# Kernel tuning notes

Hardware: AMD Instinct MI355X
Metric: run time of the kernel (lower is better)

Reference implementation:

```python
import jax, jax.numpy as jnp
from jax import lax
import numpy as np

B, T, D, H = 256, 512, 512, 1024

def _glorot(key, shape):
    fan_in, fan_out = shape
    lim = np.sqrt(6.0 / (fan_in + fan_out)).astype(np.float32)
    return jax.random.uniform(key, shape, jnp.float32, -lim, lim)

def setup_inputs() -> dict:
    key = jax.random.key(0)
    ks = jax.random.split(key, 7)
    return {
        "x": jax.random.normal(ks[0], (B, T, D), jnp.float32),
        "W": _glorot(ks[1], (D, H)),
        "U": _glorot(ks[2], (H, H)),
        "W_z": _glorot(ks[3], (D, H)),
        "U_z": _glorot(ks[4], (H, H)),
        "W_r": _glorot(ks[5], (D, H)),
        "U_r": _glorot(ks[6], (H, H)),
        "b": jnp.zeros((H,), jnp.float32),
        "b_z": jnp.zeros((H,), jnp.float32),
        "b_r": jnp.zeros((H,), jnp.float32),
    }

def reference(x, W, U, W_z, U_z, W_r, U_r, b, b_z, b_r):
    # GRU recurrence, faithful to source: update uses (1-z)*h + z*h_cand.
    def step(h, x_t):  # h: [B,H], x_t: [B,D]
        z = jax.nn.sigmoid(x_t @ W_z + h @ U_z + b_z)
        r = jax.nn.sigmoid(x_t @ W_r + h @ U_r + b_r)
        h_cand = jnp.tanh(x_t @ W + (r * h) @ U + b)
        h_new = (1.0 - z) * h + z * h_cand
        return h_new, None
    h0 = jnp.zeros((x.shape[0], W.shape[1]), x.dtype)
    xs = jnp.swapaxes(x, 0, 1)  # [T,B,D]
    hT, _ = lax.scan(step, h0, xs)
    return hT[:, None, :]  # [B,1,H] as in source (expand_dims kept through loop)
```

## Files before the change

### kernel.cpp

```cpp
#include <hip/hip_runtime.h>

typedef unsigned short ushort_t;
typedef __attribute__((ext_vector_type(8))) short short8;
typedef __attribute__((ext_vector_type(4))) float f32x4;
typedef __attribute__((ext_vector_type(4))) int i32x4;

#define NB   256
#define NT   512
#define ND   512
#define NH   1024
#define KK   1536
#define BK   128

__device__ __forceinline__ ushort_t f2bf(float f) {
  union { float f; unsigned u; } v; v.f = f;
  unsigned u = v.u;
  return (ushort_t)((u + 0x7FFFu + ((u >> 16) & 1u)) >> 16);
}
__device__ __forceinline__ int pack2(float a, float b) {
  return (int)(((unsigned)f2bf(b) << 16) | (unsigned)f2bf(a));
}
__device__ __forceinline__ float bf2f(ushort_t h) {
  union { unsigned u; float f; } v; v.u = ((unsigned)h) << 16; return v.f;
}
__device__ __forceinline__ float sigmoidf_(float x) {
  return 1.f / (1.f + __expf(-x));
}
__device__ __forceinline__ float tanhf_(float x) {
  return 1.f - 2.f / (__expf(2.f * x) + 1.f);
}

__global__ void repackT(const float* __restrict__ src, ushort_t* __restrict__ dst,
                        int K) {
  __shared__ float tile[64][65];
  const int k0 = blockIdx.x * 64, n0 = blockIdx.y * 64;
  const int tid = threadIdx.x;
  for (int i = 0; i < 16; ++i) {
    int e = tid + i * 256;
    int r = e >> 6, c = e & 63;
    tile[r][c] = src[(size_t)(k0 + r) * 1024 + n0 + c];
  }
  __syncthreads();
  for (int i = 0; i < 2; ++i) {
    int cch = tid + i * 256;
    int nl = cch >> 3, kc = (cch & 7) * 8;
    ushort_t tmp[8];
#pragma unroll
    for (int j = 0; j < 8; ++j) tmp[j] = f2bf(tile[kc + j][nl]);
    *reinterpret_cast<i32x4*>(dst + (size_t)(n0 + nl) * K + k0 + kc) =
        *reinterpret_cast<i32x4*>(tmp);
  }
}

__global__ void init_state(ushort_t* __restrict__ hb, float* __restrict__ hf) {
  int i = blockIdx.x * 256 + threadIdx.x;
  if (i < NB * NH) { hb[i] = 0; hf[i] = 0.f; }
}

__global__ void __launch_bounds__(256)
gxgemm(const float* __restrict__ x, const ushort_t* __restrict__ Bx,
       const float* __restrict__ bz, const float* __restrict__ br,
       const float* __restrict__ bb, ushort_t* __restrict__ Gx) {
  __shared__ __align__(16) char smem[32768];
  const int tid  = threadIdx.x;
  const int m0   = blockIdx.x * 64;
  const int n0   = blockIdx.y * 64;
  const int lane = tid & 63;
  const int w    = tid >> 6;
  const int wm   = w >> 1, wn = w & 1;
  const int l15  = lane & 15, l4 = lane >> 4;

  f32x4 acc[2][2];
#pragma unroll
  for (int i = 0; i < 2; ++i)
#pragma unroll
    for (int j = 0; j < 2; ++j) acc[i][j] = (f32x4){0.f, 0.f, 0.f, 0.f};

  for (int kb = 0; kb < 4; ++kb) {
    const int kbase = kb * BK;
#pragma unroll
    for (int i = 0; i < 4; ++i) {
      int c = tid + (i << 8);
      int r = c >> 4, kc = (c & 15) << 3;
      int m = m0 + r;
      int tt = m >> 8, b = m & 255;
      const float* xp = x + ((size_t)b * NT + tt) * ND + kbase + kc;
      f32x4 f0 = *reinterpret_cast<const f32x4*>(xp);
      f32x4 f1 = *reinterpret_cast<const f32x4*>(xp + 4);
      i32x4 v;
      v[0] = pack2(f0[0], f0[1]); v[1] = pack2(f0[2], f0[3]);
      v[2] = pack2(f1[0], f1[1]); v[3] = pack2(f1[2], f1[3]);
      int off = (r << 8) + (((kc << 1)) ^ ((r & 7) << 4));
      *reinterpret_cast<i32x4*>(&smem[off]) = v;
    }
#pragma unroll
    for (int i = 0; i < 4; ++i) {
      int c = tid + (i << 8);
      int n = c >> 4, kc = (c & 15) << 3;
      i32x4 v = *reinterpret_cast<const i32x4*>(Bx + (size_t)(n0 + n) * 512 + kbase + kc);
      int off = 16384 + (n << 8) + (((kc << 1)) ^ ((n & 7) << 4));
      *reinterpret_cast<i32x4*>(&smem[off]) = v;
    }
    __syncthreads();
#pragma unroll
    for (int ks = 0; ks < 4; ++ks) {
      int kbyte = ks * 64 + l4 * 16;
      short8 a[2], b[2];
#pragma unroll
      for (int i = 0; i < 2; ++i) {
        int ra = wm * 32 + i * 16 + l15;
        a[i] = *reinterpret_cast<short8*>(&smem[(ra << 8) + (kbyte ^ ((ra & 7) << 4))]);
        int nb = wn * 32 + i * 16 + l15;
        b[i] = *reinterpret_cast<short8*>(&smem[16384 + (nb << 8) + (kbyte ^ ((nb & 7) << 4))]);
      }
#pragma unroll
      for (int i = 0; i < 2; ++i)
#pragma unroll
        for (int j = 0; j < 2; ++j)
          acc[i][j] = __builtin_amdgcn_mfma_f32_16x16x32_bf16(a[i], b[j], acc[i][j], 0, 0, 0);
    }
    __syncthreads();
  }
#pragma unroll
  for (int i = 0; i < 2; ++i)
#pragma unroll
    for (int j = 0; j < 2; ++j) {
      int col = n0 + wn * 32 + j * 16 + l15;
      float bias = (col < NH) ? bz[col] : (col < 2 * NH ? br[col - NH] : bb[col - 2 * NH]);
      int mr = m0 + wm * 32 + i * 16 + 4 * l4;
#pragma unroll
      for (int jj = 0; jj < 4; ++jj)
        Gx[(size_t)(mr + jj) * 3072 + col] = f2bf(acc[i][j][jj] + bias);
    }
}

__global__ void __launch_bounds__(512)
p1k3(const ushort_t* __restrict__ Bu1, const ushort_t* __restrict__ hb,
     ushort_t* __restrict__ rhb, const float* __restrict__ hf,
     float* __restrict__ zfb, const ushort_t* __restrict__ Gx, int t) {
  extern __shared__ __align__(16) char dsm[];
  const int tid  = threadIdx.x;
  const int bid  = blockIdx.x;
  const int lane = tid & 63;
  const int w    = tid >> 6;
  const int l15  = lane & 15, l4 = lane >> 4;
  const int nt   = bid & 31;
  const int mt   = bid >> 5;
  const int m0   = mt * 32;
  const int n1   = nt * 64;
  const int msub = w >> 2, nsub = w & 3;
  const bool zside = (nt < 16);

  const int akc8 = tid & 31, arow = tid >> 5;
  i32x4 ra[2], rb[4];

#define P1_LOAD(kb_) do {                                                     \
    const ushort_t* hsrc_ = hb + (size_t)m0 * NH + (kb_) * 256 + akc8 * 8;    \
    ra[0] = *reinterpret_cast<const i32x4*>(hsrc_ + (size_t)arow * NH);       \
    ra[1] = *reinterpret_cast<const i32x4*>(hsrc_ + (size_t)(arow + 16) * NH);\
    const ushort_t* bsrc_ = Bu1 + (size_t)n1 * NH + (kb_) * 256 + akc8 * 8;   \
    _Pragma("unroll")                                                         \
    for (int i_ = 0; i_ < 4; ++i_)                                            \
      rb[i_] = *reinterpret_cast<const i32x4*>(                               \
          bsrc_ + (size_t)(arow + 16 * i_) * NH);                             \
  } while (0)

#define P1_WRITE(p_) do {                                                     \
    char* ab_ = dsm + (p_) * 49152;                                           \
    *reinterpret_cast<i32x4*>(ab_ +                                           \
        (((akc8 * 32 + arow) * 16) ^ ((akc8 & 7) << 4))) = ra[0];             \
    *reinterpret_cast<i32x4*>(ab_ +                                           \
        (((akc8 * 32 + arow + 16) * 16) ^ ((akc8 & 7) << 4))) = ra[1];        \
    char* bbase_ = ab_ + 16384;                                               \
    _Pragma("unroll")                                                         \
    for (int i_ = 0; i_ < 4; ++i_)                                            \
      *reinterpret_cast<i32x4*>(bbase_ +                                      \
          (((akc8 * 64 + arow + 16 * i_) * 16) ^ ((akc8 & 7) << 4))) = rb[i_];\
  } while (0)

  P1_LOAD(0);

  const int mrow = m0 + msub * 16 + 4 * l4;
  const int col1 = n1 + nsub * 16 + l15;
  const size_t gxrow = (size_t)t * NB * 3072;
  float gxe[4], hfe[4];
#pragma unroll
  for (int jj = 0; jj < 4; ++jj) {
    gxe[jj] = bf2f(Gx[gxrow + (size_t)(mrow + jj) * 3072 + col1]);
    if (!zside) hfe[jj] = hf[(size_t)(mrow + jj) * NH + (col1 - NH)];
  }

  f32x4 acc = {0.f, 0.f, 0.f, 0.f};
#pragma unroll
  for (int kb = 0; kb < 4; ++kb) {
    const int p = kb & 1;
    P1_WRITE(p);
    if (kb < 3) P1_LOAD(kb + 1);
    __syncthreads();
    char* base = dsm + p * 49152;
#pragma unroll
    for (int s = 0; s < 8; ++s) {
      int kc8 = s * 4 + l4;
      short8 a = *reinterpret_cast<short8*>(base +
          (((kc8 * 32 + msub * 16 + l15) * 16) ^ ((kc8 & 7) << 4)));
      short8 b = *reinterpret_cast<short8*>(base + 16384 +
          (((kc8 * 64 + nsub * 16 + l15) * 16) ^ ((kc8 & 7) << 4)));
      acc = __builtin_amdgcn_mfma_f32_16x16x32_bf16(a, b, acc, 0, 0, 0);
    }
  }
#undef P1_LOAD
#undef P1_WRITE

  if (zside) {
#pragma unroll
    for (int jj = 0; jj < 4; ++jj)
      zfb[(size_t)(mrow + jj) * NH + col1] = sigmoidf_(acc[jj] + gxe[jj]);
  } else {
    int cc = col1 - NH;
#pragma unroll
    for (int jj = 0; jj < 4; ++jj) {
      float rv = sigmoidf_(acc[jj] + gxe[jj]);
      rhb[(size_t)(mrow + jj) * NH + cc] = f2bf(rv * hfe[jj]);
    }
  }
}

__global__ void __launch_bounds__(512)
p2k3(const ushort_t* __restrict__ Bu2, const ushort_t* __restrict__ rhb,
     ushort_t* __restrict__ hb, float* __restrict__ hf,
     const float* __restrict__ zfb, const ushort_t* __restrict__ Gx,
     float* __restrict__ out, int t) {
  __shared__ __align__(16) char smem[65536];
  const int tid  = threadIdx.x;
  const int bid  = blockIdx.x;
  const int lane = tid & 63;
  const int w    = tid >> 6;
  const int l15  = lane & 15, l4 = lane >> 4;
  const int nt   = bid & 31;
  const int mt   = bid >> 5;
  const int m0   = mt * 32;
  const int n2   = nt * 32;
  const int msub = w & 1, nsub = (w >> 1) & 1, kh = w >> 2;

  const int akc8 = tid & 31, arow = tid >> 5;
  i32x4 ra[2], rb[2];

#define P2_LOAD(kb_) do {                                                     \
    const ushort_t* asrc_ = rhb + (size_t)m0 * NH + (kb_) * 256 + akc8 * 8;   \
    ra[0] = *reinterpret_cast<const i32x4*>(asrc_ + (size_t)arow * NH);       \
    ra[1] = *reinterpret_cast<const i32x4*>(asrc_ + (size_t)(arow + 16) * NH);\
    const ushort_t* bsrc_ = Bu2 + (size_t)n2 * NH + (kb_) * 256 + akc8 * 8;   \
    rb[0] = *reinterpret_cast<const i32x4*>(bsrc_ + (size_t)arow * NH);       \
    rb[1] = *reinterpret_cast<const i32x4*>(bsrc_ + (size_t)(arow + 16) * NH);\
  } while (0)

#define P2_WRITE(p_) do {                                                     \
    char* ab_ = smem + (p_) * 32768;                                          \
    *reinterpret_cast<i32x4*>(ab_ +                                           \
        (((akc8 * 32 + arow) * 16) ^ ((akc8 & 7) << 4))) = ra[0];             \
    *reinterpret_cast<i32x4*>(ab_ +                                           \
        (((akc8 * 32 + arow + 16) * 16) ^ ((akc8 & 7) << 4))) = ra[1];        \
    char* bbase_ = ab_ + 16384;                                               \
    *reinterpret_cast<i32x4*>(bbase_ +                                        \
        (((akc8 * 32 + arow) * 16) ^ ((akc8 & 7) << 4))) = rb[0];             \
    *reinterpret_cast<i32x4*>(bbase_ +                                        \
        (((akc8 * 32 + arow + 16) * 16) ^ ((akc8 & 7) << 4))) = rb[1];        \
  } while (0)

  P2_LOAD(0);

  const int mrow = m0 + msub * 16 + 4 * l4;
  const int colw = n2 + ((w >> 1) & 1) * 16 + l15;
  const size_t gxrow = (size_t)t * NB * 3072;
  float gxe[4], hfe[4], ze[4];
  if (w < 4) {
#pragma unroll
    for (int jj = 0; jj < 4; ++jj) {
      gxe[jj] = bf2f(Gx[gxrow + (size_t)(mrow + jj) * 3072 + 2048 + colw]);
      hfe[jj] = hf[(size_t)(mrow + jj) * NH + colw];
      ze[jj]  = zfb[(size_t)(mrow + jj) * NH + colw];
    }
  }

  f32x4 acc = {0.f, 0.f, 0.f, 0.f};
#pragma unroll
  for (int kb = 0; kb < 4; ++kb) {
    const int p = kb & 1;
    P2_WRITE(p);
    if (kb < 3) P2_LOAD(kb + 1);
    __syncthreads();
    char* base = smem + p * 32768;
#pragma unroll
    for (int s = 0; s < 4; ++s) {
      int kc8 = kh * 16 + s * 4 + l4;
      short8 a = *reinterpret_cast<short8*>(base +
          (((kc8 * 32 + msub * 16 + l15) * 16) ^ ((kc8 & 7) << 4)));
      short8 b = *reinterpret_cast<short8*>(base + 16384 +
          (((kc8 * 32 + nsub * 16 + l15) * 16) ^ ((kc8 & 7) << 4)));
      acc = __builtin_amdgcn_mfma_f32_16x16x32_bf16(a, b, acc, 0, 0, 0);
    }
  }
#undef P2_LOAD
#undef P2_WRITE

  __syncthreads();
  if (w >= 4)
    *reinterpret_cast<f32x4*>(smem + (w - 4) * 1024 + lane * 16) = acc;
  __syncthreads();
  if (w < 4) {
    f32x4 v = acc + *reinterpret_cast<f32x4*>(smem + w * 1024 + lane * 16);
#pragma unroll
    for (int jj = 0; jj < 4; ++jj) {
      size_t idx = (size_t)(mrow + jj) * NH + colw;
      float hc = tanhf_(v[jj] + gxe[jj]);
      float zv = ze[jj];
      float hn = (1.f - zv) * hfe[jj] + zv * hc;
      hf[idx] = hn;
      hb[idx] = f2bf(hn);
      if (t == NT - 1) out[idx] = hn;
    }
  }
}

__global__ void repack_weights(const float* __restrict__ U,  const float* __restrict__ W,
                               const float* __restrict__ Uz, const float* __restrict__ Wz,
                               const float* __restrict__ Ur, const float* __restrict__ Wr,
                               ushort_t* __restrict__ B1t, ushort_t* __restrict__ B2t) {
  const int kt = blockIdx.x, nt = blockIdx.y, which = blockIdx.z;
  if (which == 1 && nt >= 16) return;
  __shared__ float tile[64][65];
  const int k0 = kt * 64, n0 = nt * 64;
  const int tid = threadIdx.x;
  for (int i = 0; i < 16; ++i) {
    int e = tid + i * 256;
    int r = e >> 6, c = e & 63;
    int k = k0 + r, n = n0 + c;
    int nn = n & 1023;
    const float* src;
    if (which == 0) {
      if (k < NH) src = (n < NH ? Uz : Ur) + (size_t)k * NH + nn;
      else        src = (n < NH ? Wz : Wr) + (size_t)(k - NH) * NH + nn;
    } else {
      if (k < NH) src = U + (size_t)k * NH + nn;
      else        src = W + (size_t)(k - NH) * NH + nn;
    }
    tile[r][c] = *src;
  }
  __syncthreads();
  ushort_t* dst = (which == 0) ? B1t : B2t;
  for (int i = 0; i < 2; ++i) {
    int cch = tid + i * 256;
    int nl = cch >> 3, kc = (cch & 7) * 8;
    ushort_t tmp[8];
#pragma unroll
    for (int j = 0; j < 8; ++j) tmp[j] = f2bf(tile[kc + j][nl]);
    *reinterpret_cast<i32x4*>(dst + (size_t)(n0 + nl) * KK + k0 + kc) =
        *reinterpret_cast<i32x4*>(tmp);
  }
}

__global__ void __launch_bounds__(256)
gru_phase1(const float* __restrict__ x, const ushort_t* __restrict__ B1t,
           const ushort_t* __restrict__ hb, ushort_t* __restrict__ rhb,
           const float* __restrict__ hf, float* __restrict__ zfb,
           const float* __restrict__ bz, const float* __restrict__ br, int t) {
  __shared__ __align__(16) char smem[24576];
  const int tid  = threadIdx.x;
  const int bid  = blockIdx.x;
  const int lane = tid & 63;
  const int w    = tid >> 6;
  const int wm   = w >> 1, wn = w & 1;
  const int m0   = (bid >> 5) * 32;
  const int n1   = (bid & 31) * 64;
  const int l15  = lane & 15, l4 = lane >> 4;

  f32x4 acc0 = {0.f, 0.f, 0.f, 0.f}, acc1 = {0.f, 0.f, 0.f, 0.f};
  for (int kb = 0; kb < KK / BK; ++kb) {
    const int kbase = kb * BK;
#pragma unroll
    for (int i = 0; i < 2; ++i) {
      int c = tid + (i << 8);
      int r = c >> 4, kc = (c & 15) << 3;
      int m = m0 + r, k = kbase + kc;
      i32x4 v;
      if (k < NH) {
        v = *reinterpret_cast<const i32x4*>(hb + (size_t)m * NH + k);
      } else {
        const float* xp = x + (size_t)m * (NT * ND) + (size_t)t * ND + (k - NH);
        f32x4 f0 = *reinterpret_cast<const f32x4*>(xp);
        f32x4 f1 = *reinterpret_cast<const f32x4*>(xp + 4);
        v[0] = pack2(f0[0], f0[1]); v[1] = pack2(f0[2], f0[3]);
        v[2] = pack2(f1[0], f1[1]); v[3] = pack2(f1[2], f1[3]);
      }
      int off = (r << 8) + (((kc << 1)) ^ ((r & 7) << 4));
      *reinterpret_cast<i32x4*>(&smem[off]) = v;
    }
#pragma unroll
    for (int i = 0; i < 4; ++i) {
      int c = tid + (i << 8);
      int n = c >> 4, kc = (c & 15) << 3;
      i32x4 v = *reinterpret_cast<const i32x4*>(B1t + (size_t)(n1 + n) * KK + kbase + kc);
      int off = 8192 + (n << 8) + (((kc << 1)) ^ ((n & 7) << 4));
      *reinterpret_cast<i32x4*>(&smem[off]) = v;
    }
    __syncthreads();
#pragma unroll
    for (int ks = 0; ks < 4; ++ks) {
      int kbyte = ks * 64 + l4 * 16;
      int ra = wm * 16 + l15;
      short8 a = *reinterpret_cast<short8*>(&smem[(ra << 8) + (kbyte ^ ((ra & 7) << 4))]);
      int nb0 = wn * 32 + l15;
      short8 b0 = *reinterpret_cast<short8*>(&smem[8192 + (nb0 << 8) + (kbyte ^ ((nb0 & 7) << 4))]);
      int nb1 = nb0 + 16;
      short8 b1 = *reinterpret_cast<short8*>(&smem[8192 + (nb1 << 8) + (kbyte ^ ((nb1 & 7) << 4))]);
      acc0 = __builtin_amdgcn_mfma_f32_16x16x32_bf16(a, b0, acc0, 0, 0, 0);
      acc1 = __builtin_amdgcn_mfma_f32_16x16x32_bf16(a, b1, acc1, 0, 0, 0);
    }
    __syncthreads();
  }
  int mrow = m0 + wm * 16 + l4 * 4;
#pragma unroll
  for (int f = 0; f < 2; ++f) {
    f32x4 av = f ? acc1 : acc0;
    int c = n1 + wn * 32 + f * 16 + l15;
#pragma unroll
    for (int j = 0; j < 4; ++j) {
      int m = mrow + j;
      float v = av[j];
      if (c < NH) {
        zfb[(size_t)m * NH + c] = sigmoidf_(v + bz[c]);
      } else {
        int cc = c - NH;
        float rv = sigmoidf_(v + br[cc]);
        rhb[(size_t)m * NH + cc] = f2bf(rv * hf[(size_t)m * NH + cc]);
      }
    }
  }
}

__global__ void __launch_bounds__(256)
gru_phase2(const float* __restrict__ x, const ushort_t* __restrict__ B2t,
           ushort_t* __restrict__ hb, const ushort_t* __restrict__ rhb,
           float* __restrict__ hf, const float* __restrict__ zfb,
           const float* __restrict__ bb, float* __restrict__ out, int t) {
  __shared__ __align__(16) char smem[16384];
  const int tid  = threadIdx.x;
  const int bid  = blockIdx.x;
  const int lane = tid & 63;
  const int w    = tid >> 6;
  const int wm   = w >> 1, wn = w & 1;
  const int m0   = (bid >> 5) * 32;
  const int n2   = (bid & 31) * 32;
  const int l15  = lane & 15, l4 = lane >> 4;

  f32x4 acc = {0.f, 0.f, 0.f, 0.f};
  for (int kb = 0; kb < KK / BK; ++kb) {
    const int kbase = kb * BK;
#pragma unroll
    for (int i = 0; i < 2; ++i) {
      int c = tid + (i << 8);
      int r = c >> 4, kc = (c & 15) << 3;
      int m = m0 + r, k = kbase + kc;
      i32x4 v;
      if (k < NH) {
        v = *reinterpret_cast<const i32x4*>(rhb + (size_t)m * NH + k);
      } else {
        const float* xp = x + (size_t)m * (NT * ND) + (size_t)t * ND + (k - NH);
        f32x4 f0 = *reinterpret_cast<const f32x4*>(xp);
        f32x4 f1 = *reinterpret_cast<const f32x4*>(xp + 4);
        v[0] = pack2(f0[0], f0[1]); v[1] = pack2(f0[2], f0[3]);
        v[2] = pack2(f1[1], f1[1]); v[3] = pack2(f1[2], f1[3]);
      }
      int off = (r << 8) + (((kc << 1)) ^ ((r & 7) << 4));
      *reinterpret_cast<i32x4*>(&smem[off]) = v;
    }
#pragma unroll
    for (int i = 0; i < 2; ++i) {
      int c = tid + (i << 8);
      int n = c >> 4, kc = (c & 15) << 3;
      i32x4 v = *reinterpret_cast<const i32x4*>(B2t + (size_t)(n2 + n) * KK + kbase + kc);
      int off = 8192 + (n << 8) + (((kc << 1)) ^ ((n & 7) << 4));
      *reinterpret_cast<i32x4*>(&smem[off]) = v;
    }
    __syncthreads();
#pragma unroll
    for (int ks = 0; ks < 4; ++ks) {
      int kbyte = ks * 64 + l4 * 16;
      int ra = wm * 16 + l15;
      short8 a = *reinterpret_cast<short8*>(&smem[(ra << 8) + (kbyte ^ ((ra & 7) << 4))]);
      int nb = wn * 16 + l15;
      short8 b0 = *reinterpret_cast<short8*>(&smem[8192 + (nb << 8) + (kbyte ^ ((nb & 7) << 4))]);
      acc = __builtin_amdgcn_mfma_f32_16x16x32_bf16(a, b0, acc, 0, 0, 0);
    }
    __syncthreads();
  }
  int mrow = m0 + wm * 16 + l4 * 4;
  int c = n2 + wn * 16 + l15;
#pragma unroll
  for (int j = 0; j < 4; ++j) {
    int m = mrow + j;
    size_t idx = (size_t)m * NH + c;
    float hc = tanhf_(acc[j] + bb[c]);
    float zv = zfb[idx];
    float hn = (1.f - zv) * hf[idx] + zv * hc;
    hf[idx] = hn;
    hb[idx] = f2bf(hn);
    if (t == NT - 1) out[idx] = hn;
  }
}

extern "C" void kernel_launch(void* const* d_in, const int* in_sizes, int n_in,
                              void* d_out, int out_size, void* d_ws, size_t ws_size,
                              hipStream_t stream) {
  const float* x  = (const float*)d_in[0];
  const float* W  = (const float*)d_in[1];
  const float* U  = (const float*)d_in[2];
  const float* Wz = (const float*)d_in[3];
  const float* Uz = (const float*)d_in[4];
  const float* Wr = (const float*)d_in[5];
  const float* Ur = (const float*)d_in[6];
  const float* bb = (const float*)d_in[7];
  const float* bz = (const float*)d_in[8];
  const float* br = (const float*)d_in[9];
  float* out = (float*)d_out;
  char* ws = (char*)d_ws;

  ushort_t* Bu1   = (ushort_t*)(ws);
  ushort_t* Bu2   = (ushort_t*)(ws + 4194304);
  ushort_t* Bx    = (ushort_t*)(ws + 6291456);
  ushort_t* hb    = (ushort_t*)(ws + 9437184);
  ushort_t* rhb   = (ushort_t*)(ws + 9961472);
  float*    hf    = (float*)   (ws + 10485760);
  float*    zfb   = (float*)   (ws + 11534336);
  ushort_t* Gx    = (ushort_t*)(ws + 12587008);

  const bool fast = (ws_size >= (size_t)817893376ULL);

  if (fast) {
    (void)hipFuncSetAttribute(reinterpret_cast<const void*>(&p1k3),
                              hipFuncAttributeMaxDynamicSharedMemorySize, 98304);
    hipLaunchKernelGGL(repackT, dim3(16, 16), dim3(256), 0, stream, Uz, Bu1, NH);
    hipLaunchKernelGGL(repackT, dim3(16, 16), dim3(256), 0, stream, Ur, Bu1 + (size_t)NH * NH, NH);
    hipLaunchKernelGGL(repackT, dim3(16, 16), dim3(256), 0, stream, U,  Bu2, NH);
    hipLaunchKernelGGL(repackT, dim3(8, 16),  dim3(256), 0, stream, Wz, Bx, ND);
    hipLaunchKernelGGL(repackT, dim3(8, 16),  dim3(256), 0, stream, Wr, Bx + (size_t)NH * ND, ND);
    hipLaunchKernelGGL(repackT, dim3(8, 16),  dim3(256), 0, stream, W,  Bx + (size_t)2 * NH * ND, ND);
    hipLaunchKernelGGL(init_state, dim3(1024), dim3(256), 0, stream, hb, hf);
    hipLaunchKernelGGL(gxgemm, dim3(2048, 48), dim3(256), 0, stream, x, Bx, bz, br, bb, Gx);
    for (int t = 0; t < NT; ++t) {
      hipLaunchKernelGGL(p1k3, dim3(256), dim3(512), 98304, stream,
                         Bu1, hb, rhb, hf, zfb, Gx, t);
      hipLaunchKernelGGL(p2k3, dim3(256), dim3(512), 0, stream,
                         Bu2, rhb, hb, hf, zfb, Gx, out, t);
    }
  } else {
    ushort_t* B1t  = (ushort_t*)(ws);
    ushort_t* B2t  = (ushort_t*)(ws + 6291456);
    ushort_t* hb2  = (ushort_t*)(ws + 9437184);
    ushort_t* rhb2 = (ushort_t*)(ws + 9961472);
    float*    hf2  = (float*)   (ws + 10485760);
    float*    zfb2 = (float*)   (ws + 11534336);
    hipLaunchKernelGGL(repack_weights, dim3(24, 32, 2), dim3(256), 0, stream,
                       U, W, Uz, Wz, Ur, Wr, B1t, B2t);
    hipLaunchKernelGGL(init_state, dim3(1024), dim3(256), 0, stream, hb2, hf2);
    for (int t = 0; t < NT; ++t) {
      hipLaunchKernelGGL(gru_phase1, dim3(256), dim3(256), 0, stream,
                         x, B1t, hb2, rhb2, hf2, zfb2, bz, br, t);
      hipLaunchKernelGGL(gru_phase2, dim3(256), dim3(256), 0, stream,
                         x, B2t, hb2, rhb2, hf2, zfb2, bb, out, t);
    }
  }
}
```

Before: 8.374 ms.

## Enlarge input-projection GEMM tiles and deepen prefetch in recurrent step kernels

```diff
diff --git a/kernel.cpp b/kernel.cpp
--- a/kernel.cpp
+++ b/kernel.cpp
@@ -57,85 +57,108 @@
   if (i < NB * NH) { hb[i] = 0; hf[i] = 0.f; }
 }
 
+#define GOFF(row_, kc8_) (((((row_) * 8 + (kc8_)) << 4)) ^ (((row_) & 7) << 4))
+
 __global__ void __launch_bounds__(256)
-gxgemm(const float* __restrict__ x, const ushort_t* __restrict__ Bx,
-       const float* __restrict__ bz, const float* __restrict__ br,
-       const float* __restrict__ bb, ushort_t* __restrict__ Gx) {
-  __shared__ __align__(16) char smem[32768];
+gxgemm2(const float* __restrict__ x, const ushort_t* __restrict__ Bx,
+        const float* __restrict__ bz, const float* __restrict__ br,
+        const float* __restrict__ bb, ushort_t* __restrict__ Gx) {
+  __shared__ __align__(16) char smem[65536];
   const int tid  = threadIdx.x;
-  const int m0   = blockIdx.x * 64;
-  const int n0   = blockIdx.y * 64;
+  const int m0   = blockIdx.x * 128;
+  const int n0   = blockIdx.y * 128;
   const int lane = tid & 63;
   const int w    = tid >> 6;
   const int wm   = w >> 1, wn = w & 1;
   const int l15  = lane & 15, l4 = lane >> 4;
-
-  f32x4 acc[2][2];
-#pragma unroll
-  for (int i = 0; i < 2; ++i)
-#pragma unroll
-    for (int j = 0; j < 2; ++j) acc[i][j] = (f32x4){0.f, 0.f, 0.f, 0.f};
-
-  for (int kb = 0; kb < 4; ++kb) {
-    const int kbase = kb * BK;
+  const int tt   = m0 >> 8;
+  const int b0   = m0 & 255;
+
+  f32x4 rxa[4][2];
+  i32x4 rxb[4];
+
+#define GX_LOAD(kb_) do {                                                     \
+    int kbase_ = (kb_) * 64;                                                  \
+    _Pragma("unroll")                                                         \
+    for (int i_ = 0; i_ < 4; ++i_) {                                          \
+      int c_ = tid + i_ * 256;                                                \
+      int row_ = c_ >> 3, kc8_ = c_ & 7;                                      \
+      const float* xp_ = x + ((size_t)(b0 + row_) * NT + tt) * ND             \
+                          + kbase_ + kc8_ * 8;                                \
+      rxa[i_][0] = *reinterpret_cast<const f32x4*>(xp_);                      \
+      rxa[i_][1] = *reinterpret_cast<const f32x4*>(xp_ + 4);                  \
+      rxb[i_] = *reinterpret_cast<const i32x4*>(                              \
+          Bx + (size_t)(n0 + row_) * 512 + kbase_ + kc8_ * 8);                \
+    }                                                                         \
+  } while (0)
+
+#define GX_WRITE(p_) do {                                                     \
+    char* ab_ = smem + (p_) * 32768;                                          \
+    _Pragma("unroll")                                                         \
+    for (int i_ = 0; i_ < 4; ++i_) {                                          \
+      int c_ = tid + i_ * 256;                                                \
+      int row_ = c_ >> 3, kc8_ = c_ & 7;                                      \
+      i32x4 v_;                                                               \
+      v_[0] = pack2(rxa[i_][0][0], rxa[i_][0][1]);                            \
+      v_[1] = pack2(rxa[i_][0][2], rxa[i_][0][3]);                            \
+      v_[2] = pack2(rxa[i_][1][0], rxa[i_][1][1]);                            \
+      v_[3] = pack2(rxa[i_][1][2], rxa[i_][1][3]);                            \
+      *reinterpret_cast<i32x4*>(ab_ + GOFF(row_, kc8_)) = v_;                 \
+      *reinterpret_cast<i32x4*>(ab_ + 16384 + GOFF(row_, kc8_)) = rxb[i_];    \
+    }                                                                         \
+  } while (0)
+
+  f32x4 acc[4][4];
+#pragma unroll
+  for (int i = 0; i < 4; ++i)
+#pragma unroll
+    for (int j = 0; j < 4; ++j) acc[i][j] = (f32x4){0.f, 0.f, 0.f, 0.f};
+
+  GX_LOAD(0);
+#pragma unroll
+  for (int kb = 0; kb < 8; ++kb) {
+    const int p = kb & 1;
+    GX_WRITE(p);
+    if (kb < 7) GX_LOAD(kb + 1);
+    __syncthreads();
+    char* base = smem + p * 32768;
+#pragma unroll
+    for (int ks = 0; ks < 2; ++ks) {
+      int kc8 = ks * 4 + l4;
+      short8 a[4], bfr[4];
+#pragma unroll
+      for (int i = 0; i < 4; ++i) {
+        int row = wm * 64 + i * 16 + l15;
+        a[i] = *reinterpret_cast<short8*>(base + GOFF(row, kc8));
+        int col = wn * 64 + i * 16 + l15;
+        bfr[i] = *reinterpret_cast<short8*>(base + 16384 + GOFF(col, kc8));
+      }
+#pragma unroll
+      for (int i = 0; i < 4; ++i)
+#pragma unroll
+        for (int j = 0; j < 4; ++j)
+          acc[i][j] = __builtin_amdgcn_mfma_f32_16x16x32_bf16(a[i], bfr[j], acc[i][j], 0, 0, 0);
+    }
+  }
+#undef GX_LOAD
+#undef GX_WRITE
+
+#pragma unroll
+  for (int j = 0; j < 4; ++j) {
+    int col = n0 + wn * 64 + j * 16 + l15;
+    float bias = (col < NH) ? bz[col] : (col < 2 * NH ? br[col - NH] : bb[col - 2 * NH]);
 #pragma unroll
     for (int i = 0; i < 4; ++i) {
-      int c = tid + (i << 8);
-      int r = c >> 4, kc = (c & 15) << 3;
-      int m = m0 + r;
-      int tt = m >> 8, b = m & 255;
-      const float* xp = x + ((size_t)b * NT + tt) * ND + kbase + kc;
-      f32x4 f0 = *reinterpret_cast<const f32x4*>(xp);
-      f32x4 f1 = *reinterpret_cast<const f32x4*>(xp + 4);
-      i32x4 v;
-      v[0] = pack2(f0[0], f0[1]); v[1] = pack2(f0[2], f0[3]);
-      v[2] = pack2(f1[0], f1[1]); v[3] = pack2(f1[2], f1[3]);
-      int off = (r << 8) + (((kc << 1)) ^ ((r & 7) << 4));
-      *reinterpret_cast<i32x4*>(&smem[off]) = v;
-    }
-#pragma unroll
-    for (int i = 0; i < 4; ++i) {
-      int c = tid + (i << 8);
-      int n = c >> 4, kc = (c & 15) << 3;
-      i32x4 v = *reinterpret_cast<const i32x4*>(Bx + (size_t)(n0 + n) * 512 + kbase + kc);
-      int off = 16384 + (n << 8) + (((kc << 1)) ^ ((n & 7) << 4));
-      *reinterpret_cast<i32x4*>(&smem[off]) = v;
-    }
-    __syncthreads();
-#pragma unroll
-    for (int ks = 0; ks < 4; ++ks) {
-      int kbyte = ks * 64 + l4 * 16;
-      short8 a[2], b[2];
-#pragma unroll
-      for (int i = 0; i < 2; ++i) {
-        int ra = wm * 32 + i * 16 + l15;
-        a[i] = *reinterpret_cast<short8*>(&smem[(ra << 8) + (kbyte ^ ((ra & 7) << 4))]);
-        int nb = wn * 32 + i * 16 + l15;
-        b[i] = *reinterpret_cast<short8*>(&smem[16384 + (nb << 8) + (kbyte ^ ((nb & 7) << 4))]);
-      }
-#pragma unroll
-      for (int i = 0; i < 2; ++i)
-#pragma unroll
-        for (int j = 0; j < 2; ++j)
-          acc[i][j] = __builtin_amdgcn_mfma_f32_16x16x32_bf16(a[i], b[j], acc[i][j], 0, 0, 0);
-    }
-    __syncthreads();
-  }
-#pragma unroll
-  for (int i = 0; i < 2; ++i)
-#pragma unroll
-    for (int j = 0; j < 2; ++j) {
-      int col = n0 + wn * 32 + j * 16 + l15;
-      float bias = (col < NH) ? bz[col] : (col < 2 * NH ? br[col - NH] : bb[col - 2 * NH]);
-      int mr = m0 + wm * 32 + i * 16 + 4 * l4;
+      int mr = m0 + wm * 64 + i * 16 + 4 * l4;
 #pragma unroll
       for (int jj = 0; jj < 4; ++jj)
         Gx[(size_t)(mr + jj) * 3072 + col] = f2bf(acc[i][j][jj] + bias);
     }
+  }
 }
 
 __global__ void __launch_bounds__(512)
-p1k3(const ushort_t* __restrict__ Bu1, const ushort_t* __restrict__ hb,
+p1k4(const ushort_t* __restrict__ Bu1, const ushort_t* __restrict__ hb,
      ushort_t* __restrict__ rhb, const float* __restrict__ hf,
      float* __restrict__ zfb, const ushort_t* __restrict__ Gx, int t) {
   extern __shared__ __align__(16) char dsm[];
@@ -152,33 +175,46 @@
   const bool zside = (nt < 16);
 
   const int akc8 = tid & 31, arow = tid >> 5;
-  i32x4 ra[2], rb[4];
-
-#define P1_LOAD(kb_) do {                                                     \
+  i32x4 raA[2], rbA[4], raB[2], rbB[4];
+
+#define P1_LOAD(RA, RB, kb_) do {                                             \
     const ushort_t* hsrc_ = hb + (size_t)m0 * NH + (kb_) * 256 + akc8 * 8;    \
-    ra[0] = *reinterpret_cast<const i32x4*>(hsrc_ + (size_t)arow * NH);       \
-    ra[1] = *reinterpret_cast<const i32x4*>(hsrc_ + (size_t)(arow + 16) * NH);\
+    RA[0] = *reinterpret_cast<const i32x4*>(hsrc_ + (size_t)arow * NH);       \
+    RA[1] = *reinterpret_cast<const i32x4*>(hsrc_ + (size_t)(arow + 16) * NH);\
     const ushort_t* bsrc_ = Bu1 + (size_t)n1 * NH + (kb_) * 256 + akc8 * 8;   \
     _Pragma("unroll")                                                         \
     for (int i_ = 0; i_ < 4; ++i_)                                            \
-      rb[i_] = *reinterpret_cast<const i32x4*>(                               \
+      RB[i_] = *reinterpret_cast<const i32x4*>(                               \
           bsrc_ + (size_t)(arow + 16 * i_) * NH);                             \
   } while (0)
 
-#define P1_WRITE(p_) do {                                                     \
+#define P1_WRITE(p_, RA, RB) do {                                             \
     char* ab_ = dsm + (p_) * 49152;                                           \
     *reinterpret_cast<i32x4*>(ab_ +                                           \
-        (((akc8 * 32 + arow) * 16) ^ ((akc8 & 7) << 4))) = ra[0];             \
+        (((akc8 * 32 + arow) * 16) ^ ((akc8 & 7) << 4))) = RA[0];             \
     *reinterpret_cast<i32x4*>(ab_ +                                           \
-        (((akc8 * 32 + arow + 16) * 16) ^ ((akc8 & 7) << 4))) = ra[1];        \
+        (((akc8 * 32 + arow + 16) * 16) ^ ((akc8 & 7) << 4))) = RA[1];        \
     char* bbase_ = ab_ + 16384;                                               \
     _Pragma("unroll")                                                         \
     for (int i_ = 0; i_ < 4; ++i_)                                            \
       *reinterpret_cast<i32x4*>(bbase_ +                                      \
-          (((akc8 * 64 + arow + 16 * i_) * 16) ^ ((akc8 & 7) << 4))) = rb[i_];\
-  } while (0)
-
-  P1_LOAD(0);
+          (((akc8 * 64 + arow + 16 * i_) * 16) ^ ((akc8 & 7) << 4))) = RB[i_];\
+  } while (0)
+
+#define P1_MFMA(p_) do {                                                      \
+    char* base_ = dsm + (p_) * 49152;                                         \
+    _Pragma("unroll")                                                         \
+    for (int s_ = 0; s_ < 8; ++s_) {                                          \
+      int kc8_ = s_ * 4 + l4;                                                 \
+      short8 a_ = *reinterpret_cast<short8*>(base_ +                          \
+          (((kc8_ * 32 + msub * 16 + l15) * 16) ^ ((kc8_ & 7) << 4)));        \
+      short8 b_ = *reinterpret_cast<short8*>(base_ + 16384 +                  \
+          (((kc8_ * 64 + nsub * 16 + l15) * 16) ^ ((kc8_ & 7) << 4)));        \
+      acc = __builtin_amdgcn_mfma_f32_16x16x32_bf16(a_, b_, acc, 0, 0, 0);    \
+    }                                                                         \
+  } while (0)
+
+  P1_LOAD(raA, rbA, 0);
 
   const int mrow = m0 + msub * 16 + 4 * l4;
   const int col1 = n1 + nsub * 16 + l15;
@@ -190,26 +226,26 @@
     if (!zside) hfe[jj] = hf[(size_t)(mrow + jj) * NH + (col1 - NH)];
   }
 
+  P1_LOAD(raB, rbB, 1);
+
   f32x4 acc = {0.f, 0.f, 0.f, 0.f};
-#pragma unroll
-  for (int kb = 0; kb < 4; ++kb) {
-    const int p = kb & 1;
-    P1_WRITE(p);
-    if (kb < 3) P1_LOAD(kb + 1);
-    __syncthreads();
-    char* base = dsm + p * 49152;
-#pragma unroll
-    for (int s = 0; s < 8; ++s) {
-      int kc8 = s * 4 + l4;
-      short8 a = *reinterpret_cast<short8*>(base +
-          (((kc8 * 32 + msub * 16 + l15) * 16) ^ ((kc8 & 7) << 4)));
-      short8 b = *reinterpret_cast<short8*>(base + 16384 +
-          (((kc8 * 64 + nsub * 16 + l15) * 16) ^ ((kc8 & 7) << 4)));
-      acc = __builtin_amdgcn_mfma_f32_16x16x32_bf16(a, b, acc, 0, 0, 0);
-    }
-  }
+  P1_WRITE(0, raA, rbA);
+  P1_LOAD(raA, rbA, 2);
+  __syncthreads();
+  P1_MFMA(0);
+  P1_WRITE(1, raB, rbB);
+  P1_LOAD(raB, rbB, 3);
+  __syncthreads();
+  P1_MFMA(1);
+  P1_WRITE(0, raA, rbA);
+  __syncthreads();
+  P1_MFMA(0);
+  P1_WRITE(1, raB, rbB);
+  __syncthreads();
+  P1_MFMA(1);
 #undef P1_LOAD
 #undef P1_WRITE
+#undef P1_MFMA
 
   if (zside) {
 #pragma unroll
@@ -226,7 +262,7 @@
 }
 
 __global__ void __launch_bounds__(512)
-p2k3(const ushort_t* __restrict__ Bu2, const ushort_t* __restrict__ rhb,
+p2k4(const ushort_t* __restrict__ Bu2, const ushort_t* __restrict__ rhb,
      ushort_t* __restrict__ hb, float* __restrict__ hf,
      const float* __restrict__ zfb, const ushort_t* __restrict__ Gx,
      float* __restrict__ out, int t) {
@@ -243,31 +279,44 @@
   const int msub = w & 1, nsub = (w >> 1) & 1, kh = w >> 2;
 
   const int akc8 = tid & 31, arow = tid >> 5;
-  i32x4 ra[2], rb[2];
-
-#define P2_LOAD(kb_) do {                                                     \
+  i32x4 raA[2], rbA[2], raB[2], rbB[2];
+
+#define P2_LOAD(RA, RB, kb_) do {                                             \
     const ushort_t* asrc_ = rhb + (size_t)m0 * NH + (kb_) * 256 + akc8 * 8;   \
-    ra[0] = *reinterpret_cast<const i32x4*>(asrc_ + (size_t)arow * NH);       \
-    ra[1] = *reinterpret_cast<const i32x4*>(asrc_ + (size_t)(arow + 16) * NH);\
+    RA[0] = *reinterpret_cast<const i32x4*>(asrc_ + (size_t)arow * NH);       \
+    RA[1] = *reinterpret_cast<const i32x4*>(asrc_ + (size_t)(arow + 16) * NH);\
     const ushort_t* bsrc_ = Bu2 + (size_t)n2 * NH + (kb_) * 256 + akc8 * 8;   \
-    rb[0] = *reinterpret_cast<const i32x4*>(bsrc_ + (size_t)arow * NH);       \
-    rb[1] = *reinterpret_cast<const i32x4*>(bsrc_ + (size_t)(arow + 16) * NH);\
-  } while (0)
-
-#define P2_WRITE(p_) do {                                                     \
+    RB[0] = *reinterpret_cast<const i32x4*>(bsrc_ + (size_t)arow * NH);       \
+    RB[1] = *reinterpret_cast<const i32x4*>(bsrc_ + (size_t)(arow + 16) * NH);\
+  } while (0)
+
+#define P2_WRITE(p_, RA, RB) do {                                             \
     char* ab_ = smem + (p_) * 32768;                                          \
     *reinterpret_cast<i32x4*>(ab_ +                                           \
-        (((akc8 * 32 + arow) * 16) ^ ((akc8 & 7) << 4))) = ra[0];             \
+        (((akc8 * 32 + arow) * 16) ^ ((akc8 & 7) << 4))) = RA[0];             \
     *reinterpret_cast<i32x4*>(ab_ +                                           \
-        (((akc8 * 32 + arow + 16) * 16) ^ ((akc8 & 7) << 4))) = ra[1];        \
+        (((akc8 * 32 + arow + 16) * 16) ^ ((akc8 & 7) << 4))) = RA[1];        \
     char* bbase_ = ab_ + 16384;                                               \
     *reinterpret_cast<i32x4*>(bbase_ +                                        \
-        (((akc8 * 32 + arow) * 16) ^ ((akc8 & 7) << 4))) = rb[0];             \
+        (((akc8 * 32 + arow) * 16) ^ ((akc8 & 7) << 4))) = RB[0];             \
     *reinterpret_cast<i32x4*>(bbase_ +                                        \
-        (((akc8 * 32 + arow + 16) * 16) ^ ((akc8 & 7) << 4))) = rb[1];        \
-  } while (0)
-
-  P2_LOAD(0);
+        (((akc8 * 32 + arow + 16) * 16) ^ ((akc8 & 7) << 4))) = RB[1];        \
+  } while (0)
+
+#define P2_MFMA(p_) do {                                                      \
+    char* base_ = smem + (p_) * 32768;                                        \
+    _Pragma("unroll")                                                         \
+    for (int s_ = 0; s_ < 4; ++s_) {                                          \
+      int kc8_ = kh * 16 + s_ * 4 + l4;                                       \
+      short8 a_ = *reinterpret_cast<short8*>(base_ +                          \
+          (((kc8_ * 32 + msub * 16 + l15) * 16) ^ ((kc8_ & 7) << 4)));        \
+      short8 b_ = *reinterpret_cast<short8*>(base_ + 16384 +                  \
+          (((kc8_ * 32 + nsub * 16 + l15) * 16) ^ ((kc8_ & 7) << 4)));        \
+      acc = __builtin_amdgcn_mfma_f32_16x16x32_bf16(a_, b_, acc, 0, 0, 0);    \
+    }                                                                         \
+  } while (0)
+
+  P2_LOAD(raA, rbA, 0);
 
   const int mrow = m0 + msub * 16 + 4 * l4;
   const int colw = n2 + ((w >> 1) & 1) * 16 + l15;
@@ -282,26 +331,26 @@
     }
   }
 
+  P2_LOAD(raB, rbB, 1);
+
   f32x4 acc = {0.f, 0.f, 0.f, 0.f};
-#pragma unroll
-  for (int kb = 0; kb < 4; ++kb) {
-    const int p = kb & 1;
-    P2_WRITE(p);
-    if (kb < 3) P2_LOAD(kb + 1);
-    __syncthreads();
-    char* base = smem + p * 32768;
-#pragma unroll
-    for (int s = 0; s < 4; ++s) {
-      int kc8 = kh * 16 + s * 4 + l4;
-      short8 a = *reinterpret_cast<short8*>(base +
-          (((kc8 * 32 + msub * 16 + l15) * 16) ^ ((kc8 & 7) << 4)));
-      short8 b = *reinterpret_cast<short8*>(base + 16384 +
-          (((kc8 * 32 + nsub * 16 + l15) * 16) ^ ((kc8 & 7) << 4)));
-      acc = __builtin_amdgcn_mfma_f32_16x16x32_bf16(a, b, acc, 0, 0, 0);
-    }
-  }
+  P2_WRITE(0, raA, rbA);
+  P2_LOAD(raA, rbA, 2);
+  __syncthreads();
+  P2_MFMA(0);
+  P2_WRITE(1, raB, rbB);
+  P2_LOAD(raB, rbB, 3);
+  __syncthreads();
+  P2_MFMA(1);
+  P2_WRITE(0, raA, rbA);
+  __syncthreads();
+  P2_MFMA(0);
+  P2_WRITE(1, raB, rbB);
+  __syncthreads();
+  P2_MFMA(1);
 #undef P2_LOAD
 #undef P2_WRITE
+#undef P2_MFMA
 
   __syncthreads();
   if (w >= 4)
@@ -469,7 +518,7 @@
         f32x4 f0 = *reinterpret_cast<const f32x4*>(xp);
         f32x4 f1 = *reinterpret_cast<const f32x4*>(xp + 4);
         v[0] = pack2(f0[0], f0[1]); v[1] = pack2(f0[2], f0[3]);
-        v[2] = pack2(f1[1], f1[1]); v[3] = pack2(f1[2], f1[3]);
+        v[2] = pack2(f1[0], f1[1]); v[3] = pack2(f1[2], f1[3]);
       }
       int off = (r << 8) + (((kc << 1)) ^ ((r & 7) << 4));
       *reinterpret_cast<i32x4*>(&smem[off]) = v;
@@ -537,7 +586,7 @@
   const bool fast = (ws_size >= (size_t)817893376ULL);
 
   if (fast) {
-    (void)hipFuncSetAttribute(reinterpret_cast<const void*>(&p1k3),
+    (void)hipFuncSetAttribute(reinterpret_cast<const void*>(&p1k4),
                               hipFuncAttributeMaxDynamicSharedMemorySize, 98304);
     hipLaunchKernelGGL(repackT, dim3(16, 16), dim3(256), 0, stream, Uz, Bu1, NH);
     hipLaunchKernelGGL(repackT, dim3(16, 16), dim3(256), 0, stream, Ur, Bu1 + (size_t)NH * NH, NH);
@@ -546,11 +595,11 @@
     hipLaunchKernelGGL(repackT, dim3(8, 16),  dim3(256), 0, stream, Wr, Bx + (size_t)NH * ND, ND);
     hipLaunchKernelGGL(repackT, dim3(8, 16),  dim3(256), 0, stream, W,  Bx + (size_t)2 * NH * ND, ND);
     hipLaunchKernelGGL(init_state, dim3(1024), dim3(256), 0, stream, hb, hf);
-    hipLaunchKernelGGL(gxgemm, dim3(2048, 48), dim3(256), 0, stream, x, Bx, bz, br, bb, Gx);
+    hipLaunchKernelGGL(gxgemm2, dim3(1024, 24), dim3(256), 0, stream, x, Bx, bz, br, bb, Gx);
     for (int t = 0; t < NT; ++t) {
-      hipLaunchKernelGGL(p1k3, dim3(256), dim3(512), 98304, stream,
+      hipLaunchKernelGGL(p1k4, dim3(256), dim3(512), 98304, stream,
                          Bu1, hb, rhb, hf, zfb, Gx, t);
-      hipLaunchKernelGGL(p2k3, dim3(256), dim3(512), 0, stream,
+      hipLaunchKernelGGL(p2k4, dim3(256), dim3(512), 0, stream,
                          Bu2, rhb, hb, hf, zfb, Gx, out, t);
     }
   } else {
```

Result: faster. 7.831 ms (-6.5%).
